# Optimization experiments

Measured on AMD Instinct MI355X. Metric: run time of the kernel, lower is better.

## Reference

```python
import jax, jax.numpy as jnp
import numpy as np

DIM = 2048
N_HEADS = 16
N_KV_HEADS = 4
HEAD_DIM = DIM // N_HEADS  # 128
ROPE_BASE = 10000.0
QK_GAIN_INIT = 1.0
RMS_EPS = 1.1920928955078125e-07  # torch F.rms_norm default eps = finfo(fp32).eps


def _rms_norm(x):
    # normalize over last dim, no learned gain
    var = jnp.mean(jnp.square(x), axis=-1, keepdims=True)
    return x * jax.lax.rsqrt(var + RMS_EPS)


def _rope_cos_sin(seq_len, dtype):
    half = HEAD_DIM // 2
    inv_freq = 1.0 / (ROPE_BASE ** (jnp.arange(0, HEAD_DIM, 2, dtype=jnp.float32) / HEAD_DIM))
    t = jnp.arange(seq_len, dtype=jnp.float32)
    freqs = jnp.outer(t, inv_freq)  # [S, half]
    return jnp.cos(freqs).astype(dtype), jnp.sin(freqs).astype(dtype)


def _apply_rotary(x, cos, sin):
    # x: [B, H, S, D]; cos/sin: [S, D//2] broadcast over B,H
    half = x.shape[-1] // 2
    x1, x2 = x[..., :half], x[..., half:]
    return jnp.concatenate((x1 * cos + x2 * sin, x1 * (-sin) + x2 * cos), axis=-1)


def setup_inputs() -> dict:
    key = jax.random.key(0)
    ks = jax.random.split(key, 6)
    B, S = 2, 2048
    kv_dim = N_KV_HEADS * HEAD_DIM
    x = jax.random.normal(ks[0], (B, S, DIM), dtype=jnp.float32)
    Wq = jax.random.normal(ks[1], (DIM, DIM), dtype=jnp.float32) * (DIM ** -0.5)
    Wk = jax.random.normal(ks[2], (kv_dim, DIM), dtype=jnp.float32) * (DIM ** -0.5)
    Wv = jax.random.normal(ks[3], (kv_dim, DIM), dtype=jnp.float32) * (DIM ** -0.5)
    Wproj = jax.random.normal(ks[4], (DIM, DIM), dtype=jnp.float32) * (DIM ** -0.5)
    q_gain = jnp.full((N_HEADS,), QK_GAIN_INIT, dtype=jnp.float32)
    return {"x": x, "Wq": Wq, "Wk": Wk, "Wv": Wv, "Wproj": Wproj, "q_gain": q_gain}


def reference(x, Wq, Wk, Wv, Wproj, q_gain):
    B, S, D = x.shape
    G = N_HEADS // N_KV_HEADS  # GQA group size
    # QKV projections (CastedLinear, no bias)
    q = (x @ Wq.T).reshape(B, S, N_HEADS, HEAD_DIM).transpose(0, 2, 1, 3)      # [B,H,S,d]
    k = (x @ Wk.T).reshape(B, S, N_KV_HEADS, HEAD_DIM).transpose(0, 2, 1, 3)   # [B,Hkv,S,d]
    v = (x @ Wv.T).reshape(B, S, N_KV_HEADS, HEAD_DIM).transpose(0, 2, 1, 3)
    # QK RMS-norm
    q = _rms_norm(q)
    k = _rms_norm(k)
    # RoPE (scaling='none' -> attention_factor = 1.0)
    cos, sin = _rope_cos_sin(S, q.dtype)
    q = _apply_rotary(q, cos, sin)
    k = _apply_rotary(k, cos, sin)
    # per-head query gain * attention_factor (=1.0)
    q = q * q_gain.astype(q.dtype)[None, :, None, None]
    # causal GQA SDPA: group queries by kv head, no k/v materialized repeats
    qg = q.reshape(B, N_KV_HEADS, G, S, HEAD_DIM)
    scale = 1.0 / jnp.sqrt(jnp.asarray(HEAD_DIM, dtype=q.dtype))
    scores = jnp.einsum('bkgqd,bkld->bkgql', qg, k) * scale  # [B,Hkv,G,S,S]
    causal = jnp.tril(jnp.ones((S, S), dtype=bool))
    scores = jnp.where(causal, scores, jnp.asarray(-jnp.inf, dtype=scores.dtype))
    attn = jax.nn.softmax(scores, axis=-1)
    y = jnp.einsum('bkgql,bkld->bkgqd', attn, v)              # [B,Hkv,G,S,d]
    y = y.reshape(B, N_HEADS, S, HEAD_DIM).transpose(0, 2, 1, 3).reshape(B, S, D)
    return y @ Wproj.T
```

## Files before the change

### kernel.cpp

```cpp
#include <hip/hip_runtime.h>
#include <hip/hip_bf16.h>

#define DIM 2048
#define NH 16
#define NKV 4
#define HD 128
#define S_LEN 2048
#define BATCH 2
#define QKV_N 3072
#define NEGBIG -1.0e30f

typedef __attribute__((ext_vector_type(8))) short bf16x8;
typedef __attribute__((ext_vector_type(4))) float f32x4;
typedef unsigned short ushort_t;

#define GLOAD_LDS16(gp, lp)                                                       \
    __builtin_amdgcn_global_load_lds(                                             \
        (const __attribute__((address_space(1))) void*)(gp),                      \
        (__attribute__((address_space(3))) void*)(lp), 16, 0, 0)

static __device__ __forceinline__ ushort_t f2bf(float f) {
    union { float f; unsigned u; } v; v.f = f;
    unsigned r = v.u + 0x7fffu + ((v.u >> 16) & 1u);
    return (ushort_t)(r >> 16);
}
static __device__ __forceinline__ float bf2f(ushort_t u) {
    union { unsigned u; float f; } v; v.u = ((unsigned)u) << 16;
    return v.f;
}
static __device__ __forceinline__ unsigned pk2bf(float a, float b) {
    unsigned r;
    __asm__ volatile("v_cvt_pk_bf16_f32 %0, %1, %2" : "=v"(r) : "v"(a), "v"(b));
    return r;
}

__global__ __launch_bounds__(256) void cvt_bf16(const float* __restrict__ src,
                                                ushort_t* __restrict__ dst, int n) {
    int i = (blockIdx.x * 256 + threadIdx.x) * 4;
    if (i >= n) return;
    float4 v = *(const float4*)&src[i];
    uint2 o = {pk2bf(v.x, v.y), pk2bf(v.z, v.w)};
    *(uint2*)&dst[i] = o;
}

__global__ __launch_bounds__(256) void cvt_w3(const float* __restrict__ Wq,
                                              const float* __restrict__ Wk,
                                              const float* __restrict__ Wv,
                                              ushort_t* __restrict__ dst) {
    int i = (blockIdx.x * 256 + threadIdx.x) * 4;
    const float* src;
    int off;
    if (i < 4194304) { src = Wq; off = i; }
    else if (i < 5242880) { src = Wk; off = i - 4194304; }
    else { src = Wv; off = i - 5242880; }
    float4 v = *(const float4*)&src[off];
    uint2 o = {pk2bf(v.x, v.y), pk2bf(v.z, v.w)};
    *(uint2*)&dst[i] = o;
}

static __device__ __forceinline__ void store_c(float* p, float v) { *p = v; }
static __device__ __forceinline__ void store_c(ushort_t* p, float v) { *p = f2bf(v); }

template <typename OutT>
__global__ __launch_bounds__(256) void gemm_bt(const ushort_t* __restrict__ A,
                                               const ushort_t* __restrict__ B,
                                               OutT* __restrict__ C,
                                               int M, int N, int K) {
    __shared__ __align__(16) ushort_t As[2][128 * 32];
    __shared__ __align__(16) ushort_t Bs[2][128 * 32];
    const int t = threadIdx.x;
    const int lane = t & 63;
    const int wave = t >> 6;
    const int m16 = lane & 15;
    const int quad = lane >> 4;
    const int wr = wave >> 1;
    const int wc = wave & 1;
    const int m0 = blockIdx.y * 128;
    const int n0 = blockIdx.x * 128;

    f32x4 acc[4][4];
#pragma unroll
    for (int i = 0; i < 4; i++)
#pragma unroll
        for (int j = 0; j < 4; j++) acc[i][j] = (f32x4){0.f, 0.f, 0.f, 0.f};

    const int r0 = t >> 2;
    const int c8 = (t & 3) * 8;

#pragma unroll
    for (int half = 0; half < 2; ++half) {
        GLOAD_LDS16(&A[(size_t)(m0 + half * 64 + r0) * K + c8],
                    &As[0][(half * 64 + wave * 16) * 32]);
        GLOAD_LDS16(&B[(size_t)(n0 + half * 64 + r0) * K + c8],
                    &Bs[0][(half * 64 + wave * 16) * 32]);
    }
    for (int k0 = 0; k0 < K; k0 += 32) {
        const int cur = (k0 >> 5) & 1;
        __syncthreads();
        if (k0 + 32 < K) {
#pragma unroll
            for (int half = 0; half < 2; ++half) {
                GLOAD_LDS16(&A[(size_t)(m0 + half * 64 + r0) * K + k0 + 32 + c8],
                            &As[cur ^ 1][(half * 64 + wave * 16) * 32]);
                GLOAD_LDS16(&B[(size_t)(n0 + half * 64 + r0) * K + k0 + 32 + c8],
                            &Bs[cur ^ 1][(half * 64 + wave * 16) * 32]);
            }
        }
        bf16x8 af[4], bfr[4];
#pragma unroll
        for (int mt = 0; mt < 4; mt++)
            af[mt] = *(const bf16x8*)&As[cur][(wr * 64 + mt * 16 + m16) * 32 + quad * 8];
#pragma unroll
        for (int nt = 0; nt < 4; nt++)
            bfr[nt] = *(const bf16x8*)&Bs[cur][(wc * 64 + nt * 16 + m16) * 32 + quad * 8];
#pragma unroll
        for (int mt = 0; mt < 4; mt++)
#pragma unroll
            for (int nt = 0; nt < 4; nt++)
                acc[mt][nt] = __builtin_amdgcn_mfma_f32_16x16x32_bf16(af[mt], bfr[nt],
                                                                      acc[mt][nt], 0, 0, 0);
    }
#pragma unroll
    for (int mt = 0; mt < 4; mt++) {
#pragma unroll
        for (int r = 0; r < 4; r++) {
            int row = m0 + wr * 64 + mt * 16 + quad * 4 + r;
#pragma unroll
            for (int nt = 0; nt < 4; nt++) {
                int col = n0 + wc * 64 + nt * 16 + m16;
                store_c(&C[(size_t)row * N + col], acc[mt][nt][r]);
            }
        }
    }
}

__global__ __launch_bounds__(256) void rope_qk(ushort_t* __restrict__ qkv,
                                               const float* __restrict__ gain) {
    const int wave = threadIdx.x >> 6, lane = threadIdx.x & 63;
    int r = blockIdx.x * 4 + wave;
    ushort_t* p;
    float g;
    int s;
    if (r < 65536) {
        const int h = r & (NH - 1);
        const int bs = r >> 4;
        s = bs & (S_LEN - 1);
        p = qkv + (size_t)bs * QKV_N + h * HD;
        g = gain[h];
    } else {
        r -= 65536;
        const int kv = r & (NKV - 1);
        const int bs = r >> 2;
        s = bs & (S_LEN - 1);
        p = qkv + (size_t)bs * QKV_N + DIM + kv * HD;
        g = 1.0f;
    }
    float x1 = bf2f(p[lane]);
    float x2 = bf2f(p[lane + 64]);
    float ss = x1 * x1 + x2 * x2;
#pragma unroll
    for (int m = 32; m >= 1; m >>= 1) ss += __shfl_xor(ss, m, 64);
    float rms = rsqrtf(ss * (1.0f / 128.0f) + 1.1920928955078125e-07f);
    x1 *= rms; x2 *= rms;
    float invf = powf(10000.0f, -(float)lane * (1.0f / 64.0f));
    float fr = (float)s * invf;
    float c = cosf(fr), sn = sinf(fr);
    p[lane] = f2bf((x1 * c + x2 * sn) * g);
    p[lane + 64] = f2bf((x2 * c - x1 * sn) * g);
}

__global__ __launch_bounds__(256) void vtrans(const ushort_t* __restrict__ qkv,
                                              ushort_t* __restrict__ vt) {
    __shared__ ushort_t tile[64][72];
    const int s0 = blockIdx.x * 64, d0 = blockIdx.y * 64;
    const int kv = blockIdx.z & (NKV - 1), b = blockIdx.z >> 2;
    const int t = threadIdx.x;
    const int r = t >> 2, cg = (t & 3) * 16;
    const ushort_t* src = qkv + ((size_t)(b * S_LEN + s0 + r)) * QKV_N + (DIM + NKV * HD) +
                          kv * HD + d0 + cg;
    *(uint4*)&tile[r][cg] = *(const uint4*)&src[0];
    *(uint4*)&tile[r][cg + 8] = *(const uint4*)&src[8];
    __syncthreads();
    ushort_t ov[16];
#pragma unroll
    for (int j = 0; j < 16; j++) ov[j] = tile[cg + j][r];
    ushort_t* dst = vt + ((size_t)((b * NKV + kv) * HD + d0 + r)) * S_LEN + s0 + cg;
    *(uint4*)&dst[0] = *(uint4*)&ov[0];
    *(uint4*)&dst[8] = *(uint4*)&ov[8];
}

__device__ __constant__ short attn_tab[24][4] = {
    {15, 0, 16, 14}, {15, 16, 32, 15}, {7, 0, 16, -1}, {14, 0, 15, 12},
    {13, 0, 14, 10}, {13, 14, 28, 11}, {6, 0, 14, -1}, {10, 0, 11, 4},
    {12, 0, 13, 8},  {12, 13, 26, 9}, {14, 15, 30, 13}, {11, 0, 12, 6},
    {11, 12, 24, 7}, {5, 0, 12, -1}, {10, 11, 22, 5},  {9, 0, 10, 2},
    {2, 0, 6, -1},   {1, 0, 4, -1},  {0, 0, 2, -1},    {3, 0, 8, -1},
    {8, 0, 9, 0},    {8, 9, 18, 1},  {9, 10, 20, 3},   {4, 0, 10, -1},
};

__global__ __launch_bounds__(256) void attn(const ushort_t* __restrict__ QKV,
                                            const ushort_t* __restrict__ Vt,
                                            ushort_t* __restrict__ Y,
                                            ushort_t* __restrict__ Po,
                                            float* __restrict__ Pl) {
    __shared__ __align__(16) ushort_t Ks[64 * 128];
    __shared__ __align__(16) ushort_t Vs[128 * 64];
    __shared__ __align__(16) ushort_t Ps[4][32 * 72];
    const int lane = threadIdx.x & 63;
    const int wave = threadIdx.x >> 6;
    const int m16 = lane & 15, quad = lane >> 4;
    const int seg = blockIdx.x >> 5;
    const int hb = blockIdx.x & 31;
    const int h = hb & (NH - 1), b = hb >> 4;
    const int kvh = h >> 2;
    const int bx = attn_tab[seg][0];
    const int t0 = attn_tab[seg][1];
    const int t1 = attn_tab[seg][2];
    const int slotl = attn_tab[seg][3];
    const int q0w = bx * 128 + wave * 32;

    const ushort_t* kbase = QKV + (size_t)b * S_LEN * QKV_N + DIM + kvh * HD;
    const ushort_t* vbase = Vt + (size_t)(b * NKV + kvh) * (HD * S_LEN);

    bf16x8 bq[2][4];
#pragma unroll
    for (int g = 0; g < 2; g++)
#pragma unroll
        for (int ks = 0; ks < 4; ks++)
            bq[g][ks] = *(const bf16x8*)&QKV[((size_t)(b * S_LEN + q0w + g * 16 + m16)) * QKV_N +
                                             h * HD + ks * 32 + quad * 8];

    float ls[2] = {0.f, 0.f};
    f32x4 o[2][8];
#pragma unroll
    for (int g = 0; g < 2; g++)
#pragma unroll
        for (int nd = 0; nd < 8; nd++) o[g][nd] = (f32x4){0.f, 0.f, 0.f, 0.f};

    ushort_t* pw = Ps[wave];
    for (int t = t0; t < t1; ++t) {
        const int kv0 = t * 64;
        __syncthreads();
#pragma unroll
        for (int i = 0; i < 4; i++) {
            const int c0 = i * 256 + wave * 64;
            const int ck = c0 + lane;
            const int krow = ck >> 4;
            const int kcol = (ck & 15) ^ (krow & 7);
            GLOAD_LDS16(kbase + (size_t)(kv0 + krow) * QKV_N + kcol * 8, &Ks[c0 * 8]);
            const int vd = ck >> 3;
            const int vcol = (ck & 7) ^ (vd & 7);
            GLOAD_LDS16(vbase + (size_t)vd * S_LEN + kv0 + vcol * 8, &Vs[c0 * 8]);
        }
        __syncthreads();

        f32x4 st[2][4];
#pragma unroll
        for (int g = 0; g < 2; g++)
#pragma unroll
            for (int nt = 0; nt < 4; nt++) st[g][nt] = (f32x4){0.f, 0.f, 0.f, 0.f};
#pragma unroll
        for (int ks = 0; ks < 4; ks++)
#pragma unroll
            for (int nt = 0; nt < 4; nt++) {
                const int row = nt * 16 + m16;
                bf16x8 ak = *(const bf16x8*)&Ks[row * 128 + (((ks * 4 + quad) ^ (row & 7)) * 8)];
#pragma unroll
                for (int g = 0; g < 2; g++)
                    st[g][nt] = __builtin_amdgcn_mfma_f32_16x16x32_bf16(ak, bq[g][ks],
                                                                        st[g][nt], 0, 0, 0);
            }
#pragma unroll
        for (int g = 0; g < 2; g++) {
            const int q0g = q0w + g * 16;
            const int qg = q0g + m16;
            const bool interior = (kv0 + 63 <= q0g);
            float rs = 0.f;
#pragma unroll
            for (int nt = 0; nt < 4; nt++) {
                float p[4];
#pragma unroll
                for (int r = 0; r < 4; r++) {
                    float x = st[g][nt][r] * 0.08838834764831845f;
                    if (!interior) {
                        const int kg = kv0 + nt * 16 + quad * 4 + r;
                        x = (kg > qg) ? NEGBIG : x;
                    }
                    p[r] = __expf(x);
                }
                rs += (p[0] + p[1]) + (p[2] + p[3]);
                uint2 pk = {pk2bf(p[0], p[1]), pk2bf(p[2], p[3])};
                *(uint2*)&pw[(g * 16 + m16) * 72 + nt * 16 + quad * 4] = pk;
            }
            ls[g] += rs;
        }
        __asm__ __volatile__("s_waitcnt lgkmcnt(0)" ::: "memory");
        bf16x8 bp[2][2];
#pragma unroll
        for (int g = 0; g < 2; g++)
#pragma unroll
            for (int kk = 0; kk < 2; kk++)
                bp[g][kk] = *(const bf16x8*)&pw[(g * 16 + m16) * 72 + kk * 32 + quad * 8];
#pragma unroll
        for (int kk = 0; kk < 2; kk++)
#pragma unroll
            for (int nd = 0; nd < 8; nd++) {
                const int vrow = nd * 16 + m16;
                bf16x8 av = *(const bf16x8*)&Vs[vrow * 64 + (((kk * 4 + quad) ^ (vrow & 7)) * 8)];
#pragma unroll
                for (int g = 0; g < 2; g++)
                    o[g][nd] = __builtin_amdgcn_mfma_f32_16x16x32_bf16(av, bp[g][kk],
                                                                       o[g][nd], 0, 0, 0);
            }
    }
    float l_tot[2];
#pragma unroll
    for (int g = 0; g < 2; g++) {
        float v = ls[g];
        v += __shfl_xor(v, 16, 64);
        v += __shfl_xor(v, 32, 64);
        l_tot[g] = v;
    }
    if (slotl < 0) {
#pragma unroll
        for (int g = 0; g < 2; g++) {
            const float inv = 1.0f / l_tot[g];
            const int qg = q0w + g * 16 + m16;
            ushort_t* yp = Y + ((size_t)(b * S_LEN + qg)) * DIM + h * HD;
#pragma unroll
            for (int nd = 0; nd < 8; nd++) {
                uint2 pk = {pk2bf(o[g][nd][0] * inv, o[g][nd][1] * inv),
                            pk2bf(o[g][nd][2] * inv, o[g][nd][3] * inv)};
                *(uint2*)&yp[nd * 16 + quad * 4] = pk;
            }
        }
    } else {
        const int slot = ((b * NH + h) << 4) + slotl;
        ushort_t* po = Po + (size_t)slot * (128 * 128);
#pragma unroll
        for (int g = 0; g < 2; g++) {
            const int ql = wave * 32 + g * 16 + m16;
#pragma unroll
            for (int nd = 0; nd < 8; nd++) {
                uint2 pk = {pk2bf(o[g][nd][0], o[g][nd][1]),
                            pk2bf(o[g][nd][2], o[g][nd][3])};
                *(uint2*)&po[ql * 128 + nd * 16 + quad * 4] = pk;
            }
            if (quad == 0) Pl[slot * 128 + ql] = l_tot[g];
        }
    }
}

__global__ __launch_bounds__(256) void attn_combine(const ushort_t* __restrict__ Po,
                                                    const float* __restrict__ Pl,
                                                    ushort_t* __restrict__ Y) {
    const int R = blockIdx.x * 2 + (threadIdx.x >> 7);
    const int d = threadIdx.x & 127;
    const int q = R & 127;
    const int bx8 = (R >> 7) & 7;
    const int h = (R >> 10) & 15;
    const int b = R >> 14;
    const int slot0 = ((b * NH + h) << 4) + bx8 * 2;
    const float l0 = Pl[slot0 * 128 + q], l1 = Pl[(slot0 + 1) * 128 + q];
    const float inv = 1.0f / (l0 + l1);
    const float o0 = bf2f(Po[(size_t)slot0 * (128 * 128) + q * 128 + d]);
    const float o1 = bf2f(Po[(size_t)(slot0 + 1) * (128 * 128) + q * 128 + d]);
    const int qg = (bx8 + 8) * 128 + q;
    Y[((size_t)(b * S_LEN + qg)) * DIM + h * HD + d] = f2bf((o0 + o1) * inv);
}

extern "C" void kernel_launch(void* const* d_in, const int* in_sizes, int n_in,
                              void* d_out, int out_size, void* d_ws, size_t ws_size,
                              hipStream_t stream) {
    (void)in_sizes; (void)n_in; (void)out_size; (void)ws_size;
    const float* xf  = (const float*)d_in[0];
    const float* Wqf = (const float*)d_in[1];
    const float* Wkf = (const float*)d_in[2];
    const float* Wvf = (const float*)d_in[3];
    const float* Wpf = (const float*)d_in[4];
    const float* gn  = (const float*)d_in[5];
    float* out = (float*)d_out;

    char* ws = (char*)d_ws;
    ushort_t* xb    = (ushort_t*)(ws);
    ushort_t* qkv   = (ushort_t*)(ws + (16ull << 20));
    ushort_t* vt    = (ushort_t*)(ws + (40ull << 20));
    ushort_t* Wqkvb = (ushort_t*)(ws + (44ull << 20));
    ushort_t* Wpb   = (ushort_t*)(ws + (56ull << 20));
    ushort_t* y     = xb;
    ushort_t* Po    = (ushort_t*)(ws + (44ull << 20));
    float*    Pl    = (float*)(ws + (60ull << 20));

    const int M = BATCH * S_LEN;
    cvt_bf16<<<dim3(M * DIM / 1024), 256, 0, stream>>>(xf, xb, M * DIM);
    cvt_w3<<<dim3(QKV_N * DIM / 1024), 256, 0, stream>>>(Wqf, Wkf, Wvf, Wqkvb);
    gemm_bt<<<dim3(QKV_N / 128, M / 128), 256, 0, stream>>>(xb, Wqkvb, qkv, M, QKV_N, DIM);
    rope_qk<<<dim3(M * (NH + NKV) / 4), 256, 0, stream>>>(qkv, gn);
    vtrans<<<dim3(S_LEN / 64, HD / 64, BATCH * NKV), 256, 0, stream>>>(qkv, vt);
    attn<<<dim3(768, 1, 1), 256, 0, stream>>>(qkv, vt, y, Po, Pl);
    attn_combine<<<dim3(BATCH * NH * 8 * 128 / 2), 256, 0, stream>>>(Po, Pl, y);
    cvt_bf16<<<dim3(DIM * DIM / 1024), 256, 0, stream>>>(Wpf, Wpb, DIM * DIM);
    gemm_bt<<<dim3(DIM / 128, M / 128), 256, 0, stream>>>(y, Wpb, out, M, DIM, DIM);
}
```

Before: 333.5 us.

## Double-buffer K/V tiles in attention and fuse input conversion kernels

The attention kernel now keeps two LDS buffers for K and V and issues the global-to-LDS loads for the next tile before computing on the current one, so load latency can overlap the MFMA work. The P scratch buffer drops its padding in favour of an XOR swizzle to avoid bank conflicts. The x and Wqkv fp32-to-bf16 conversions are merged into one launch, and the RoPE frequency powf is replaced with exp2f. Doubling the K/V buffers raises LDS use per block, which can lower occupancy.

```diff
diff --git a/kernel.cpp b/kernel.cpp
--- a/kernel.cpp
+++ b/kernel.cpp
@@ -34,26 +34,35 @@
     return r;
 }
 
+__global__ __launch_bounds__(256) void cvt_in(const float* __restrict__ x,
+                                              const float* __restrict__ Wq,
+                                              const float* __restrict__ Wk,
+                                              const float* __restrict__ Wv,
+                                              ushort_t* __restrict__ xb,
+                                              ushort_t* __restrict__ Wqkvb) {
+    int i = (blockIdx.x * 256 + threadIdx.x) * 4;
+    const float* src;
+    ushort_t* dst;
+    int soff, doff;
+    if (i < 8388608) {
+        src = x; dst = xb; soff = i; doff = i;
+    } else {
+        int j = i - 8388608;
+        dst = Wqkvb; doff = j;
+        if (j < 4194304) { src = Wq; soff = j; }
+        else if (j < 5242880) { src = Wk; soff = j - 4194304; }
+        else { src = Wv; soff = j - 5242880; }
+    }
+    float4 v = *(const float4*)&src[soff];
+    uint2 o = {pk2bf(v.x, v.y), pk2bf(v.z, v.w)};
+    *(uint2*)&dst[doff] = o;
+}
+
 __global__ __launch_bounds__(256) void cvt_bf16(const float* __restrict__ src,
                                                 ushort_t* __restrict__ dst, int n) {
     int i = (blockIdx.x * 256 + threadIdx.x) * 4;
     if (i >= n) return;
     float4 v = *(const float4*)&src[i];
-    uint2 o = {pk2bf(v.x, v.y), pk2bf(v.z, v.w)};
-    *(uint2*)&dst[i] = o;
-}
-
-__global__ __launch_bounds__(256) void cvt_w3(const float* __restrict__ Wq,
-                                              const float* __restrict__ Wk,
-                                              const float* __restrict__ Wv,
-                                              ushort_t* __restrict__ dst) {
-    int i = (blockIdx.x * 256 + threadIdx.x) * 4;
-    const float* src;
-    int off;
-    if (i < 4194304) { src = Wq; off = i; }
-    else if (i < 5242880) { src = Wk; off = i - 4194304; }
-    else { src = Wv; off = i - 5242880; }
-    float4 v = *(const float4*)&src[off];
     uint2 o = {pk2bf(v.x, v.y), pk2bf(v.z, v.w)};
     *(uint2*)&dst[i] = o;
 }
@@ -162,7 +171,7 @@
     for (int m = 32; m >= 1; m >>= 1) ss += __shfl_xor(ss, m, 64);
     float rms = rsqrtf(ss * (1.0f / 128.0f) + 1.1920928955078125e-07f);
     x1 *= rms; x2 *= rms;
-    float invf = powf(10000.0f, -(float)lane * (1.0f / 64.0f));
+    float invf = exp2f(-0.20762050593046f * (float)lane);
     float fr = (float)s * invf;
     float c = cosf(fr), sn = sinf(fr);
     p[lane] = f2bf((x1 * c + x2 * sn) * g);
@@ -203,9 +212,9 @@
                                             ushort_t* __restrict__ Y,
                                             ushort_t* __restrict__ Po,
                                             float* __restrict__ Pl) {
-    __shared__ __align__(16) ushort_t Ks[64 * 128];
-    __shared__ __align__(16) ushort_t Vs[128 * 64];
-    __shared__ __align__(16) ushort_t Ps[4][32 * 72];
+    __shared__ __align__(16) ushort_t Ks[2][64 * 128];
+    __shared__ __align__(16) ushort_t Vs[2][128 * 64];
+    __shared__ __align__(16) ushort_t Ps[4][32 * 64];
     const int lane = threadIdx.x & 63;
     const int wave = threadIdx.x >> 6;
     const int m16 = lane & 15, quad = lane >> 4;
@@ -222,37 +231,45 @@
     const ushort_t* kbase = QKV + (size_t)b * S_LEN * QKV_N + DIM + kvh * HD;
     const ushort_t* vbase = Vt + (size_t)(b * NKV + kvh) * (HD * S_LEN);
 
-    bf16x8 bq[2][4];
-#pragma unroll
-    for (int g = 0; g < 2; g++)
-#pragma unroll
-        for (int ks = 0; ks < 4; ks++)
-            bq[g][ks] = *(const bf16x8*)&QKV[((size_t)(b * S_LEN + q0w + g * 16 + m16)) * QKV_N +
-                                             h * HD + ks * 32 + quad * 8];
-
-    float ls[2] = {0.f, 0.f};
-    f32x4 o[2][8];
-#pragma unroll
-    for (int g = 0; g < 2; g++)
-#pragma unroll
-        for (int nd = 0; nd < 8; nd++) o[g][nd] = (f32x4){0.f, 0.f, 0.f, 0.f};
-
-    ushort_t* pw = Ps[wave];
-    for (int t = t0; t < t1; ++t) {
-        const int kv0 = t * 64;
-        __syncthreads();
+    auto stage = [&](int tt, int buf) {
+        const int kv0 = tt * 64;
 #pragma unroll
         for (int i = 0; i < 4; i++) {
             const int c0 = i * 256 + wave * 64;
             const int ck = c0 + lane;
             const int krow = ck >> 4;
             const int kcol = (ck & 15) ^ (krow & 7);
-            GLOAD_LDS16(kbase + (size_t)(kv0 + krow) * QKV_N + kcol * 8, &Ks[c0 * 8]);
+            GLOAD_LDS16(kbase + (size_t)(kv0 + krow) * QKV_N + kcol * 8, &Ks[buf][c0 * 8]);
             const int vd = ck >> 3;
             const int vcol = (ck & 7) ^ (vd & 7);
-            GLOAD_LDS16(vbase + (size_t)vd * S_LEN + kv0 + vcol * 8, &Vs[c0 * 8]);
-        }
+            GLOAD_LDS16(vbase + (size_t)vd * S_LEN + kv0 + vcol * 8, &Vs[buf][c0 * 8]);
+        }
+    };
+
+    bf16x8 bq[2][4];
+#pragma unroll
+    for (int g = 0; g < 2; g++)
+#pragma unroll
+        for (int ks = 0; ks < 4; ks++)
+            bq[g][ks] = *(const bf16x8*)&QKV[((size_t)(b * S_LEN + q0w + g * 16 + m16)) * QKV_N +
+                                             h * HD + ks * 32 + quad * 8];
+
+    float ls[2] = {0.f, 0.f};
+    f32x4 o[2][8];
+#pragma unroll
+    for (int g = 0; g < 2; g++)
+#pragma unroll
+        for (int nd = 0; nd < 8; nd++) o[g][nd] = (f32x4){0.f, 0.f, 0.f, 0.f};
+
+    ushort_t* pw = Ps[wave];
+    const int sw = m16 & 7;
+
+    stage(t0, 0);
+    for (int t = t0; t < t1; ++t) {
+        const int buf = (t - t0) & 1;
+        const int kv0 = t * 64;
         __syncthreads();
+        if (t + 1 < t1) stage(t + 1, buf ^ 1);
 
         f32x4 st[2][4];
 #pragma unroll
@@ -264,7 +281,8 @@
 #pragma unroll
             for (int nt = 0; nt < 4; nt++) {
                 const int row = nt * 16 + m16;
-                bf16x8 ak = *(const bf16x8*)&Ks[row * 128 + (((ks * 4 + quad) ^ (row & 7)) * 8)];
+                bf16x8 ak = *(const bf16x8*)&Ks[buf][row * 128 +
+                                                    (((ks * 4 + quad) ^ (row & 7)) * 8)];
 #pragma unroll
                 for (int g = 0; g < 2; g++)
                     st[g][nt] = __builtin_amdgcn_mfma_f32_16x16x32_bf16(ak, bq[g][ks],
@@ -290,7 +308,8 @@
                 }
                 rs += (p[0] + p[1]) + (p[2] + p[3]);
                 uint2 pk = {pk2bf(p[0], p[1]), pk2bf(p[2], p[3])};
-                *(uint2*)&pw[(g * 16 + m16) * 72 + nt * 16 + quad * 4] = pk;
+                *(uint2*)&pw[(g * 16 + m16) * 64 +
+                             (((nt * 2 + (quad >> 1)) ^ sw) * 8) + (quad & 1) * 4] = pk;
             }
             ls[g] += rs;
         }
@@ -300,13 +319,15 @@
         for (int g = 0; g < 2; g++)
 #pragma unroll
             for (int kk = 0; kk < 2; kk++)
-                bp[g][kk] = *(const bf16x8*)&pw[(g * 16 + m16) * 72 + kk * 32 + quad * 8];
+                bp[g][kk] = *(const bf16x8*)&pw[(g * 16 + m16) * 64 +
+                                                (((kk * 4 + quad) ^ sw) * 8)];
 #pragma unroll
         for (int kk = 0; kk < 2; kk++)
 #pragma unroll
             for (int nd = 0; nd < 8; nd++) {
                 const int vrow = nd * 16 + m16;
-                bf16x8 av = *(const bf16x8*)&Vs[vrow * 64 + (((kk * 4 + quad) ^ (vrow & 7)) * 8)];
+                bf16x8 av = *(const bf16x8*)&Vs[buf][vrow * 64 +
+                                                     (((kk * 4 + quad) ^ (vrow & 7)) * 8)];
 #pragma unroll
                 for (int g = 0; g < 2; g++)
                     o[g][nd] = __builtin_amdgcn_mfma_f32_16x16x32_bf16(av, bp[g][kk],
@@ -392,8 +413,8 @@
     float*    Pl    = (float*)(ws + (60ull << 20));
 
     const int M = BATCH * S_LEN;
-    cvt_bf16<<<dim3(M * DIM / 1024), 256, 0, stream>>>(xf, xb, M * DIM);
-    cvt_w3<<<dim3(QKV_N * DIM / 1024), 256, 0, stream>>>(Wqf, Wkf, Wvf, Wqkvb);
+    cvt_in<<<dim3((M * DIM + QKV_N * DIM) / 1024), 256, 0, stream>>>(xf, Wqf, Wkf, Wvf,
+                                                                     xb, Wqkvb);
     gemm_bt<<<dim3(QKV_N / 128, M / 128), 256, 0, stream>>>(xb, Wqkvb, qkv, M, QKV_N, DIM);
     rope_qk<<<dim3(M * (NH + NKV) / 4), 256, 0, stream>>>(qkv, gn);
     vtrans<<<dim3(S_LEN / 64, HD / 64, BATCH * NKV), 256, 0, stream>>>(qkv, vt);
```

Result: no change. 329.8 us (-1.1%).
